# Performance work log

Measured on AMD Instinct MI355X. Metric: run time of the kernel, lower is better.

## Reference

```python
import jax, jax.numpy as jnp
import numpy as np

B, C, H, W = 2, 192, 128, 128
HEADS = 4
M = 128          # num_tokens
RD = 10          # reducted_dim
GS = 256         # category_size
TDF = 16         # dim_ffn_td
HID = 4 * C      # mlp hidden (768)
HIDT = HID + TDF # 784 after concat with token-dict features
KS = 5


def _ln(x, g, b):
    mu = x.mean(-1, keepdims=True)
    var = ((x - mu) ** 2).mean(-1, keepdims=True)
    return (x - mu) / jnp.sqrt(var + 1e-5) * g + b


def _gelu(x):
    return jax.nn.gelu(x, approximate=False)  # torch nn.GELU default = exact erf


def setup_inputs() -> dict:
    key = jax.random.key(0)
    ks = jax.random.split(key, 16)
    s = 0.02
    inp = {
        "x": jax.random.normal(ks[0], (B, C, H, W), jnp.float32),
        "x_size": H,
        "td": jax.random.normal(ks[1], (M, C), jnp.float32),
        "g1": jnp.ones((C,)), "b1": jnp.zeros((C,)),
        "g2": jnp.ones((C,)), "b2": jnp.zeros((C,)),
        "g3": jnp.ones((C,)), "b3": jnp.zeros((C,)),
        "wq_w": jax.random.normal(ks[2], (C, RD)) * s, "wq_b": jnp.zeros((RD,)),
        "wk_w": jax.random.normal(ks[3], (C, RD)) * s, "wk_b": jnp.zeros((RD,)),
        "wv_w": jax.random.normal(ks[4], (C, C)) * s, "wv_b": jnp.zeros((C,)),
        "ca_scale": jnp.ones((1,)),
        "wqkv_w": jax.random.normal(ks[5], (C, 3 * C)) * s, "wqkv_b": jnp.zeros((3 * C,)),
        "proj_w": jax.random.normal(ks[6], (C, C)) * s, "proj_b": jnp.zeros((C,)),
        "fc_td_w": jax.random.normal(ks[7], (C, TDF)) * s, "fc_td_b": jnp.zeros((TDF,)),
        "fc1_w": jax.random.normal(ks[8], (C, HID)) * s, "fc1_b": jnp.zeros((HID,)),
        "dw_w": jax.random.normal(ks[9], (HIDT, 1, KS, KS)) * s, "dw_b": jnp.zeros((HIDT,)),
        "fc2_w": jax.random.normal(ks[10], (HIDT, C)) * s, "fc2_b": jnp.zeros((C,)),
    }
    return inp


def reference(x, x_size, td, g1, b1, g2, b2, g3, b3, wq_w, wq_b, wk_w, wk_b,
              wv_w, wv_b, ca_scale, wqkv_w, wqkv_b, proj_w, proj_b,
              fc_td_w, fc_td_b, fc1_w, fc1_b, dw_w, dw_b, fc2_w, fc2_b):
    b, c, h, w = x.shape
    n = h * w
    xs = x.reshape(b, c, n).transpose(0, 2, 1)          # [b,n,c] patch_embed
    shortcut = xs
    xn = _ln(xs, g1, b1)                                # norm1

    # ---- ATD_CA: L2-normalized cross-attention to token dict ----
    q = xn @ wq_w + wq_b                                # [b,n,rd]
    k = td @ wk_w + wk_b                                # [m,rd]
    v = td @ wv_w + wv_b                                # [m,c]
    qn = q / jnp.maximum(jnp.linalg.norm(q, axis=-1, keepdims=True), 1e-12)
    kn = k / jnp.maximum(jnp.linalg.norm(k, axis=-1, keepdims=True), 1e-12)
    sim = jnp.einsum('bnr,mr->bnm', qn, kn)
    scale = 1.0 + jnp.clip(ca_scale, 0.0, 3.0) * np.log(M)
    sim = jax.nn.softmax(sim * scale, axis=-1)          # [b,n,m]
    x_atd = jnp.einsum('bnm,mc->bnc', sim, v)
    tk_id = jnp.argmax(sim, axis=-1)                    # [b,n] int

    # ---- AC_MSA: category-sorted grouped self-attention ----
    qkv = xn @ wqkv_w + wqkv_b                          # [b,n,3c]
    sort_idx = jnp.argsort(tk_id, axis=-1)              # [b,n]
    inv_idx = jnp.argsort(sort_idx, axis=-1)            # index_reverse
    shuf = jnp.take_along_axis(qkv, sort_idx[:, :, None], axis=1)
    gs = min(n, GS)
    ng = (n + gs - 1) // gs
    pad_n = ng * gs - n
    pad = jnp.flip(shuf[:, n - pad_n:n, :], axis=1)
    padded = jnp.concatenate([shuf, pad], axis=1)       # [b, ng*gs, 3c]
    hd = c // HEADS
    y = padded.reshape(b, ng, gs, 3, HEADS, hd)
    y = jnp.transpose(y, (3, 0, 1, 4, 2, 5))            # [3,b,ng,H,gs,hd]
    q2, k2, v2 = y[0], y[1], y[2]
    attn = jnp.einsum('bghqd,bghkd->bghqk', q2, k2) * (hd ** -0.5)
    attn = jax.nn.softmax(attn, axis=-1)
    o = jnp.einsum('bghqk,bghkd->bghqd', attn, v2)
    o = jnp.transpose(o, (0, 1, 3, 2, 4)).reshape(b, ng * gs, c)[:, :n, :]
    o = jnp.take_along_axis(o, inv_idx[:, :, None], axis=1)
    x_aca = o @ proj_w + proj_b

    # ---- token-dict features gathered per token ----
    td_feat = td @ fc_td_w + fc_td_b                    # [m,tdf]
    x_td = jnp.take(td_feat, tk_id, axis=0)             # [b,n,tdf]

    # ---- ConvFFN_td ----
    xn2 = _ln(xs, g2, b2)
    h1 = _gelu(xn2 @ fc1_w + fc1_b)                     # [b,n,hid]
    hcat = jnp.concatenate([h1, x_td], axis=-1)         # [b,n,hidt]
    img = hcat.transpose(0, 2, 1).reshape(b, HIDT, h, w)
    conv = jax.lax.conv_general_dilated(
        img, dw_w, window_strides=(1, 1), padding=((KS // 2, KS // 2),) * 2,
        dimension_numbers=('NCHW', 'OIHW', 'NCHW'), feature_group_count=HIDT)
    conv = _gelu(conv + dw_b[None, :, None, None])
    conv = conv.reshape(b, HIDT, n).transpose(0, 2, 1)
    x_ffn = (hcat + conv) @ fc2_w + fc2_b
    x_ffn = _ln(x_ffn, g3, b3)                          # norm3

    out = shortcut + x_atd + x_aca + x_ffn
    return out.transpose(0, 2, 1).reshape(b, c, h, w)
```

## Files before the change

kernel.cpp:

```cpp
#include <hip/hip_runtime.h>
#include <hip/hip_bf16.h>
#include <math.h>

using bf16 = __hip_bfloat16;

static constexpr int B = 2, C = 192, Hh = 128, Ww = 128, N = Hh * Ww;
static constexpr int M = 128, RD = 10, GS = 256, NG = N / GS;
static constexpr int HEADS = 4, HD = C / HEADS;
static constexpr int TDF = 16, HID = 4 * C, HIDT = HID + TDF;
static constexpr int TC3 = 3 * C;
static constexpr float LOG_M = 4.852030263919617f;
static constexpr float ATT_SCALE = 0.14433756729740643f;

typedef __attribute__((ext_vector_type(8))) short bf16x8;
typedef __attribute__((ext_vector_type(4))) float f32x4;

__device__ __forceinline__ float b2f(bf16 v) { return __bfloat162float(v); }
__device__ __forceinline__ bf16 f2b(float v) { return __float2bfloat16(v); }
__device__ __forceinline__ float bits2f(unsigned short u) { return __uint_as_float(((unsigned)u) << 16); }
__device__ __forceinline__ unsigned short f2bits(float f) {
    union { bf16 h; unsigned short u; } cv; cv.h = f2b(f); return cv.u;
}
__device__ __forceinline__ float gelu_exact(float v) {
    return 0.5f * v * (1.0f + erff(v * 0.70710678118654752f));
}

__global__ void __launch_bounds__(256) k_wtrans(const float* in, bf16* out, int K, int Nn) {
    __shared__ float T[64][65];
    int n0 = blockIdx.x * 64, k0 = blockIdx.y * 64;
    int tid = threadIdx.x;
    for (int e = tid; e < 4096; e += 256) {
        int kk = e >> 6, nn = e & 63;
        if (k0 + kk < K) T[kk][nn] = in[(size_t)(k0 + kk) * Nn + n0 + nn];
    }
    __syncthreads();
    for (int e = tid; e < 4096; e += 256) {
        int nn = e >> 6, kk = e & 63;
        if (k0 + kk < K) out[(size_t)(n0 + nn) * K + k0 + kk] = f2b(T[kk][nn]);
    }
}

__global__ void k_precompute(const float* td, const float* wk_w, const float* wk_b,
                             const float* wv_w, const float* wv_b,
                             const float* fc_td_w, const float* fc_td_b,
                             float* kn, bf16* vvT, float* tdf) {
    int m = blockIdx.x;
    int lane = threadIdx.x;
    __shared__ float trow[C];
    for (int ch = lane; ch < C; ch += 64) trow[ch] = td[m * C + ch];
    __syncthreads();
    __shared__ float ks[RD];
    __shared__ float inv_s;
    if (lane < RD) {
        float s = wk_b[lane];
        for (int ch = 0; ch < C; ++ch) s += trow[ch] * wk_w[ch * RD + lane];
        ks[lane] = s;
    }
    __syncthreads();
    if (lane == 0) {
        float ss = 0.f;
        for (int r = 0; r < RD; ++r) ss += ks[r] * ks[r];
        inv_s = 1.0f / fmaxf(sqrtf(ss), 1e-12f);
    }
    __syncthreads();
    if (lane < RD) kn[m * RD + lane] = ks[lane] * inv_s;
    for (int c0 = 0; c0 < 3; ++c0) {
        int co = lane + 64 * c0;
        float s = wv_b[co];
        for (int ch = 0; ch < C; ++ch) s += trow[ch] * wv_w[ch * C + co];
        vvT[(size_t)co * M + m] = f2b(s);
    }
    if (lane < TDF) {
        float s = fc_td_b[lane];
        for (int ch = 0; ch < C; ++ch) s += trow[ch] * fc_td_w[ch * TDF + lane];
        tdf[m * TDF + lane] = s;
    }
}

__global__ void __launch_bounds__(256) k_ln(const float* x, const float* g1, const float* b1,
                                            const float* g2, const float* b2v,
                                            bf16* xn1, bf16* xn2, float* xn32, float* acc) {
    __shared__ float Xs[64 * 193];
    __shared__ float mu_s[64], rs_s[64];
    int tid = threadIdx.x;
    int m0 = blockIdx.x * 64;
    int b = m0 / N, i0 = m0 % N;
    for (int e = tid; e < 192 * 64; e += 256) {
        int ch = e >> 6, ii = e & 63;
        Xs[ii * 193 + ch] = x[((size_t)b * C + ch) * N + i0 + ii];
    }
    __syncthreads();
    {
        int tok = tid >> 2, part = tid & 3;
        float s = 0.f, ss = 0.f;
        for (int ch = part * 48; ch < part * 48 + 48; ++ch) {
            float v = Xs[tok * 193 + ch]; s += v; ss += v * v;
        }
        s += __shfl_xor(s, 1); ss += __shfl_xor(ss, 1);
        s += __shfl_xor(s, 2); ss += __shfl_xor(ss, 2);
        if (part == 0) {
            float mu = s / C;
            mu_s[tok] = mu;
            rs_s[tok] = rsqrtf(ss / C - mu * mu + 1e-5f);
        }
    }
    __syncthreads();
    for (int e = tid; e < 64 * 192; e += 256) {
        int ii = e / 192, ch = e % 192;
        float v = Xs[ii * 193 + ch];
        float xn = (v - mu_s[ii]) * rs_s[ii];
        size_t g = (size_t)(m0 + ii);
        xn1[g * C + ch] = f2b(xn * g1[ch] + b1[ch]);
        xn2[g * C + ch] = f2b(xn * g2[ch] + b2v[ch]);
        xn32[g * C + ch] = xn;
        acc[g * C + ch] = v;
    }
}

__global__ void __launch_bounds__(256) k_atdca(const float* xn32, const float* g1, const float* b1,
                        const float* wq_w, const float* wq_b, const float* ca_scale,
                        const float* kn, bf16* p_buf, int* tk_id) {
    int t0 = blockIdx.x * 4;
    int w = threadIdx.x >> 6, lane = threadIdx.x & 63;
    int g = t0 + w;
    float xn[3];
    #pragma unroll
    for (int k = 0; k < 3; ++k) {
        int ch = lane + 64 * k;
        xn[k] = xn32[(size_t)g * C + ch] * g1[ch] + b1[ch];
    }
    float q[RD];
    #pragma unroll
    for (int r = 0; r < RD; ++r) {
        float p = 0.f;
        #pragma unroll
        for (int k = 0; k < 3; ++k) { int ch = lane + 64 * k; p += xn[k] * wq_w[ch * RD + r]; }
        for (int mk = 32; mk >= 1; mk >>= 1) p += __shfl_xor(p, mk);
        q[r] = p + wq_b[r];
    }
    float ssn = 0.f;
    #pragma unroll
    for (int r = 0; r < RD; ++r) ssn += q[r] * q[r];
    float invq = 1.0f / fmaxf(sqrtf(ssn), 1e-12f);
    float s0 = 0.f, s1 = 0.f;
    #pragma unroll
    for (int r = 0; r < RD; ++r) {
        float qr = q[r] * invq;
        s0 += qr * kn[lane * RD + r];
        s1 += qr * kn[(lane + 64) * RD + r];
    }
    float mv; int mi;
    if (s1 > s0) { mv = s1; mi = lane + 64; } else { mv = s0; mi = lane; }
    for (int mk = 32; mk >= 1; mk >>= 1) {
        float ov = __shfl_xor(mv, mk); int oi = __shfl_xor(mi, mk);
        if (ov > mv || (ov == mv && oi < mi)) { mv = ov; mi = oi; }
    }
    float cs = ca_scale[0]; cs = fminf(fmaxf(cs, 0.0f), 3.0f);
    float scale = 1.0f + cs * LOG_M;
    float e0 = expf((s0 - mv) * scale), e1 = expf((s1 - mv) * scale);
    float sum = e0 + e1;
    for (int mk = 32; mk >= 1; mk >>= 1) sum += __shfl_xor(sum, mk);
    float invs = 1.0f / sum;
    p_buf[(size_t)g * M + lane] = f2b(e0 * invs);
    p_buf[(size_t)g * M + lane + 64] = f2b(e1 * invs);
    if (lane == 0) tk_id[g] = mi;
}

__global__ void __launch_bounds__(256) k_pv(const bf16* p_buf, const bf16* vvT, float* acc) {
    __shared__ __align__(16) short As[64 * 136];
    __shared__ __align__(16) short Bs[64 * 136];
    int tid = threadIdx.x;
    int m0 = blockIdx.x * 64;
    int n0 = blockIdx.y * 64;
    for (int e = tid; e < 64 * 16; e += 256) {
        int m = e >> 4, kc = (e & 15) * 8;
        *(uint4*)&As[m * 136 + kc] = *(const uint4*)(p_buf + (size_t)(m0 + m) * M + kc);
    }
    for (int e = tid; e < 64 * 16; e += 256) {
        int n = e >> 4, kc = (e & 15) * 8;
        *(uint4*)&Bs[n * 136 + kc] = *(const uint4*)(vvT + (size_t)(n0 + n) * M + kc);
    }
    __syncthreads();
    int w = tid >> 6, lane = tid & 63;
    int wm = (w >> 1) * 32, wn = (w & 1) * 32;
    int lr = lane & 15, lk = (lane >> 4) * 8;
    f32x4 acc00 = {0.f,0.f,0.f,0.f}, acc01 = acc00, acc10 = acc00, acc11 = acc00;
    #pragma unroll
    for (int ks = 0; ks < 4; ++ks) {
        int k0 = ks * 32 + lk;
        bf16x8 a0 = *(bf16x8*)&As[(wm + lr) * 136 + k0];
        bf16x8 a1 = *(bf16x8*)&As[(wm + 16 + lr) * 136 + k0];
        bf16x8 b0 = *(bf16x8*)&Bs[(wn + lr) * 136 + k0];
        bf16x8 b1 = *(bf16x8*)&Bs[(wn + 16 + lr) * 136 + k0];
        acc00 = __builtin_amdgcn_mfma_f32_16x16x32_bf16(a0, b0, acc00, 0, 0, 0);
        acc01 = __builtin_amdgcn_mfma_f32_16x16x32_bf16(a0, b1, acc01, 0, 0, 0);
        acc10 = __builtin_amdgcn_mfma_f32_16x16x32_bf16(a1, b0, acc10, 0, 0, 0);
        acc11 = __builtin_amdgcn_mfma_f32_16x16x32_bf16(a1, b1, acc11, 0, 0, 0);
    }
    int rbase = (lane >> 4) * 4;
    f32x4 accs[2][2] = {{acc00, acc01}, {acc10, acc11}};
    #pragma unroll
    for (int mt = 0; mt < 2; ++mt) {
        #pragma unroll
        for (int nt = 0; nt < 2; ++nt) {
            int co = n0 + wn + nt * 16 + lr;
            #pragma unroll
            for (int r = 0; r < 4; ++r) {
                int tok = m0 + wm + mt * 16 + rbase + r;
                acc[(size_t)tok * C + co] += accs[mt][nt][r];
            }
        }
    }
}

template<int OUTLD, int MODE>
__global__ void __launch_bounds__(256) k_gemm_big(const bf16* Abuf, const bf16* Wt, const float* bias,
                                                  bf16* outb, float* outf) {
    __shared__ __align__(16) unsigned short As[128 * 104];
    __shared__ __align__(16) unsigned short Bs[96 * 104];
    int tid = threadIdx.x;
    int m0 = blockIdx.x * 128, n0 = blockIdx.y * 96;
    int w = tid >> 6, lane = tid & 63;
    int wm = (w >> 1) * 64, wn = (w & 1) * 48;
    int lr = lane & 15, g8 = lane >> 4;
    f32x4 acc[4][3];
    #pragma unroll
    for (int mt = 0; mt < 4; ++mt)
        #pragma unroll
        for (int nt = 0; nt < 3; ++nt) acc[mt][nt] = (f32x4){0.f,0.f,0.f,0.f};
    for (int kc = 0; kc < 2; ++kc) {
        int kb = kc * 96;
        __syncthreads();
        for (int e = tid; e < 128 * 12; e += 256) {
            int m = e / 12, blk = e % 12;
            *(uint4*)&As[m * 104 + blk * 8] = *(const uint4*)(Abuf + (size_t)(m0 + m) * C + kb + blk * 8);
        }
        for (int e = tid; e < 96 * 12; e += 256) {
            int n = e / 12, blk = e % 12;
            *(uint4*)&Bs[n * 104 + blk * 8] = *(const uint4*)(Wt + (size_t)(n0 + n) * C + kb + blk * 8);
        }
        __syncthreads();
        #pragma unroll
        for (int ks = 0; ks < 3; ++ks) {
            int blk = ks * 4 + g8;
            bf16x8 a[4];
            bf16x8 bfr[3];
            #pragma unroll
            for (int mt = 0; mt < 4; ++mt) a[mt] = *(bf16x8*)&As[(wm + mt * 16 + lr) * 104 + blk * 8];
            #pragma unroll
            for (int nt = 0; nt < 3; ++nt) bfr[nt] = *(bf16x8*)&Bs[(wn + nt * 16 + lr) * 104 + blk * 8];
            #pragma unroll
            for (int mt = 0; mt < 4; ++mt)
                #pragma unroll
                for (int nt = 0; nt < 3; ++nt)
                    acc[mt][nt] = __builtin_amdgcn_mfma_f32_16x16x32_bf16(a[mt], bfr[nt], acc[mt][nt], 0, 0, 0);
        }
    }
    #pragma unroll
    for (int nt = 0; nt < 3; ++nt) {
        int co = n0 + wn + nt * 16 + lr;
        float bv = bias[co];
        #pragma unroll
        for (int mt = 0; mt < 4; ++mt) {
            #pragma unroll
            for (int r = 0; r < 4; ++r) {
                int tok = m0 + wm + mt * 16 + g8 * 4 + r;
                float v = acc[mt][nt][r] + bv;
                if (MODE == 0) outb[(size_t)tok * OUTLD + co] = f2b(v);
                else if (MODE == 1) outb[(size_t)tok * OUTLD + co] = f2b(gelu_exact(v));
                else outf[(size_t)tok * OUTLD + co] += v;
            }
        }
    }
}

__global__ void k_sort_count(const int* tk_id, int* chunk_cnt) {
    int c = blockIdx.x, b = blockIdx.y;
    int tid = threadIdx.x;
    __shared__ int cnt[M];
    cnt[tid] = 0;
    __syncthreads();
    atomicAdd(&cnt[tk_id[b * N + c * 128 + tid]], 1);
    __syncthreads();
    chunk_cnt[(b * 128 + c) * M + tid] = cnt[tid];
}

__global__ void k_sort_scan(int* chunk_cnt) {
    int b = blockIdx.x;
    int k = threadIdx.x;
    int tot = 0;
    for (int c = 0; c < 128; ++c) tot += chunk_cnt[(b * 128 + c) * M + k];
    __shared__ int totals[M];
    __shared__ int base[M];
    totals[k] = tot;
    __syncthreads();
    if (k == 0) {
        int run = 0;
        for (int kk = 0; kk < M; ++kk) { base[kk] = run; run += totals[kk]; }
    }
    __syncthreads();
    int run = base[k];
    for (int c = 0; c < 128; ++c) {
        int v = chunk_cnt[(b * 128 + c) * M + k];
        chunk_cnt[(b * 128 + c) * M + k] = run;
        run += v;
    }
}

__global__ void k_sort_scatter(const int* tk_id, const int* chunk_cnt, int* sort_idx) {
    int c = blockIdx.x, b = blockIdx.y;
    int k = threadIdx.x;
    __shared__ int keys[128];
    keys[k] = tk_id[b * N + c * 128 + k];
    __syncthreads();
    int off = chunk_cnt[(b * 128 + c) * M + k];
    for (int j = 0; j < 128; ++j) {
        if (keys[j] == k) sort_idx[b * N + off++] = c * 128 + j;
    }
}

__global__ void __launch_bounds__(256) k_attn_mfma(const bf16* qkv, const int* sort_idx, bf16* o_buf) {
    int g = blockIdx.x, h = blockIdx.y, b = blockIdx.z;
    __shared__ int sidx[GS];
    __shared__ __align__(16) unsigned short Kl[256 * 64];
    __shared__ __align__(16) unsigned short Vt[48 * 256];
    __shared__ __align__(16) unsigned short Pl[4][64 * 32];
    int tid = threadIdx.x;
    sidx[tid] = sort_idx[b * N + g * GS + tid];
    __syncthreads();
    {
        int row = tid;
        int srow = sidx[row];
        size_t kb = ((size_t)(b * N + srow)) * TC3 + C + h * HD;
        size_t vb = ((size_t)(b * N + srow)) * TC3 + 2 * C + h * HD;
        #pragma unroll
        for (int db = 0; db < 6; ++db) {
            uint4 kv = *(const uint4*)(qkv + kb + db * 8);
            *(uint4*)&Kl[row * 64 + ((db ^ (row & 7)) * 8)] = kv;
            uint4 vv4 = *(const uint4*)(qkv + vb + db * 8);
            unsigned short* vu = (unsigned short*)&vv4;
            #pragma unroll
            for (int j = 0; j < 8; ++j) {
                int d = db * 8 + j;
                Vt[d * 256 + (((row >> 3) ^ (d & 7)) * 8) + (row & 7)] = vu[j];
            }
        }
        uint4 z = {0u,0u,0u,0u};
        *(uint4*)&Kl[row * 64 + ((6 ^ (row & 7)) * 8)] = z;
        *(uint4*)&Kl[row * 64 + ((7 ^ (row & 7)) * 8)] = z;
    }
    __syncthreads();
    int w = tid >> 6, l = tid & 63;
    int lq = l & 15, g8 = l >> 4;
    bf16x8 qf[4][2];
    #pragma unroll
    for (int qt = 0; qt < 4; ++qt) {
        int qrow = sidx[w * 64 + qt * 16 + lq];
        size_t qb = ((size_t)(b * N + qrow)) * TC3 + h * HD;
        qf[qt][0] = *(const bf16x8*)(qkv + qb + g8 * 8);
        int d1 = 32 + g8 * 8;
        if (d1 < HD) qf[qt][1] = *(const bf16x8*)(qkv + qb + d1);
        else { uint4 z = {0u,0u,0u,0u}; qf[qt][1] = *(bf16x8*)&z; }
    }
    float mrun[4], lrun[4];
    f32x4 Oa[4][3];
    #pragma unroll
    for (int qt = 0; qt < 4; ++qt) {
        mrun[qt] = -1e30f; lrun[qt] = 0.f;
        #pragma unroll
        for (int dt = 0; dt < 3; ++dt) Oa[qt][dt] = (f32x4){0.f,0.f,0.f,0.f};
    }
    unsigned short* Pw = &Pl[w][0];
    for (int ck = 0; ck < 8; ++ck) {
        int kbase = ck * 32;
        bf16x8 kf[2][2];
        #pragma unroll
        for (int kt = 0; kt < 2; ++kt) {
            int key = kbase + kt * 16 + lq;
            #pragma unroll
            for (int ks = 0; ks < 2; ++ks)
                kf[kt][ks] = *(bf16x8*)&Kl[key * 64 + (((ks * 4 + g8) ^ (key & 7)) * 8)];
        }
        bf16x8 vf[3];
        #pragma unroll
        for (int dt = 0; dt < 3; ++dt) {
            int d = dt * 16 + lq;
            vf[dt] = *(bf16x8*)&Vt[d * 256 + ((((kbase >> 3) + g8) ^ (d & 7)) * 8)];
        }
        #pragma unroll
        for (int qt = 0; qt < 4; ++qt) {
            f32x4 s0 = {0.f,0.f,0.f,0.f}, s1 = s0;
            s0 = __builtin_amdgcn_mfma_f32_16x16x32_bf16(kf[0][0], qf[qt][0], s0, 0, 0, 0);
            s0 = __builtin_amdgcn_mfma_f32_16x16x32_bf16(kf[0][1], qf[qt][1], s0, 0, 0, 0);
            s1 = __builtin_amdgcn_mfma_f32_16x16x32_bf16(kf[1][0], qf[qt][0], s1, 0, 0, 0);
            s1 = __builtin_amdgcn_mfma_f32_16x16x32_bf16(kf[1][1], qf[qt][1], s1, 0, 0, 0);
            float sv0[4], sv1[4];
            float cmax = -1e30f;
            #pragma unroll
            for (int r = 0; r < 4; ++r) {
                sv0[r] = s0[r] * ATT_SCALE; sv1[r] = s1[r] * ATT_SCALE;
                cmax = fmaxf(cmax, fmaxf(sv0[r], sv1[r]));
            }
            cmax = fmaxf(cmax, __shfl_xor(cmax, 16));
            cmax = fmaxf(cmax, __shfl_xor(cmax, 32));
            float mnew = fmaxf(mrun[qt], cmax);
            float sf = expf(mrun[qt] - mnew);
            float p0[4], p1[4], csum = 0.f;
            #pragma unroll
            for (int r = 0; r < 4; ++r) {
                p0[r] = expf(sv0[r] - mnew); p1[r] = expf(sv1[r] - mnew);
                csum += p0[r] + p1[r];
            }
            csum += __shfl_xor(csum, 16);
            csum += __shfl_xor(csum, 32);
            lrun[qt] = lrun[qt] * sf + csum;
            mrun[qt] = mnew;
            int q = qt * 16 + lq;
            {
                unsigned short pw[4];
                #pragma unroll
                for (int r = 0; r < 4; ++r) pw[r] = f2bits(p0[r]);
                int slot = g8;
                int addr = q * 32 + (((slot >> 1) ^ (q & 3)) * 8) + (slot & 1) * 4;
                *(uint2*)&Pw[addr] = *(uint2*)pw;
                #pragma unroll
                for (int r = 0; r < 4; ++r) pw[r] = f2bits(p1[r]);
                slot = 4 + g8;
                addr = q * 32 + (((slot >> 1) ^ (q & 3)) * 8) + (slot & 1) * 4;
                *(uint2*)&Pw[addr] = *(uint2*)pw;
            }
            float sfr[4];
            #pragma unroll
            for (int r = 0; r < 4; ++r) sfr[r] = __shfl(sf, 4 * g8 + r);
            #pragma unroll
            for (int dt = 0; dt < 3; ++dt)
                #pragma unroll
                for (int r = 0; r < 4; ++r) Oa[qt][dt][r] *= sfr[r];
            bf16x8 pa = *(bf16x8*)&Pw[q * 32 + ((g8 ^ (lq & 3)) * 8)];
            #pragma unroll
            for (int dt = 0; dt < 3; ++dt)
                Oa[qt][dt] = __builtin_amdgcn_mfma_f32_16x16x32_bf16(pa, vf[dt], Oa[qt][dt], 0, 0, 0);
        }
    }
    #pragma unroll
    for (int qt = 0; qt < 4; ++qt) {
        float invq = 1.0f / lrun[qt];
        float invr[4];
        #pragma unroll
        for (int r = 0; r < 4; ++r) invr[r] = __shfl(invq, 4 * g8 + r);
        #pragma unroll
        for (int r = 0; r < 4; ++r) {
            int grow = sidx[w * 64 + qt * 16 + 4 * g8 + r];
            size_t obase = ((size_t)(b * N + grow)) * C + h * HD;
            #pragma unroll
            for (int dt = 0; dt < 3; ++dt)
                o_buf[obase + dt * 16 + lq] = f2b(Oa[qt][dt][r] * invr[r]);
        }
    }
}

__global__ void k_tdfill(const int* tk_id, const float* tdf, bf16* hcat) {
    int idx = blockIdx.x * 256 + threadIdx.x;
    if (idx >= B * N * TDF) return;
    int tok = idx >> 4, f = idx & 15;
    hcat[(size_t)tok * HIDT + HID + f] = f2b(tdf[tk_id[tok] * TDF + f]);
}

__global__ void __launch_bounds__(256) k_conv(const bf16* hcat, const float* dw_w, const float* dw_b,
                                              bf16* convsum) {
    int st = blockIdx.x;
    int c16 = blockIdx.y;
    int b = blockIdx.z;
    int tx0 = (st & 7) * 16, ty0 = (st >> 3) * 16;
    int tid = threadIdx.x;
    __shared__ __align__(16) float Hf[20 * 81 * 4];
    __shared__ __align__(16) float Wf[25 * 16];
    __shared__ float Wb[16];
    for (int e = tid; e < 400; e += 256) {
        int tap = e >> 4, ch = e & 15;
        Wf[e] = dw_w[(size_t)(c16 * 16 + ch) * 25 + tap];
    }
    if (tid < 16) Wb[tid] = dw_b[c16 * 16 + tid];
    for (int e = tid; e < 800; e += 256) {
        int pos = e >> 1, sc = e & 1;
        int py = pos / 20, px = pos % 20;
        int gy = ty0 + py - 2, gx = tx0 + px - 2;
        uint4 v = {0u, 0u, 0u, 0u};
        if (gy >= 0 && gy < Hh && gx >= 0 && gx < Ww)
            v = *(const uint4*)(hcat + ((size_t)b * N + gy * Ww + gx) * HIDT + c16 * 16 + sc * 8);
        unsigned short* u = (unsigned short*)&v;
        float4 f0 = { bits2f(u[0]), bits2f(u[1]), bits2f(u[2]), bits2f(u[3]) };
        float4 f1 = { bits2f(u[4]), bits2f(u[5]), bits2f(u[6]), bits2f(u[7]) };
        int base = (py * 81 + px * 4 + sc * 2) * 4;
        *(float4*)&Hf[base] = f0;
        *(float4*)&Hf[base + 4] = f1;
    }
    __syncthreads();
    int cc = tid & 1, lx = (tid >> 1) & 7, ly = tid >> 4;
    float acc[2][8] = {};
    #pragma unroll 1
    for (int ky = 0; ky < 5; ++ky) {
        int py = ly + ky;
        float4 w[5][2];
        #pragma unroll
        for (int kx = 0; kx < 5; ++kx) {
            w[kx][0] = *(float4*)&Wf[(ky * 5 + kx) * 16 + cc * 8];
            w[kx][1] = *(float4*)&Wf[(ky * 5 + kx) * 16 + cc * 8 + 4];
        }
        #pragma unroll
        for (int c = 0; c < 6; ++c) {
            int px = 2 * lx + c;
            int base = (py * 81 + px * 4 + cc * 2) * 4;
            float4 f0 = *(float4*)&Hf[base];
            float4 f1 = *(float4*)&Hf[base + 4];
            float f[8] = { f0.x, f0.y, f0.z, f0.w, f1.x, f1.y, f1.z, f1.w };
            #pragma unroll
            for (int kx = 0; kx < 5; ++kx) {
                int ox = c - kx;
                if (ox >= 0 && ox < 2) {
                    const float* wp = (const float*)&w[kx][0];
                    #pragma unroll
                    for (int j = 0; j < 8; ++j) acc[ox][j] += f[j] * wp[j];
                }
            }
        }
    }
    int gy = ty0 + ly;
    #pragma unroll
    for (int ox = 0; ox < 2; ++ox) {
        int px = 2 * lx + ox + 2, py = ly + 2;
        int base = (py * 81 + px * 4 + cc * 2) * 4;
        float4 f0 = *(float4*)&Hf[base];
        float4 f1 = *(float4*)&Hf[base + 4];
        float cf[8] = { f0.x, f0.y, f0.z, f0.w, f1.x, f1.y, f1.z, f1.w };
        unsigned short ow[8];
        #pragma unroll
        for (int j = 0; j < 8; ++j)
            ow[j] = f2bits(cf[j] + gelu_exact(acc[ox][j] + Wb[cc * 8 + j]));
        int gx = tx0 + 2 * lx + ox;
        *(uint4*)(convsum + ((size_t)b * N + gy * Ww + gx) * HIDT + c16 * 16 + cc * 8) = *(uint4*)ow;
    }
}

__global__ void __launch_bounds__(256) k_fc2ln(const bf16* convsum, const bf16* Wt,
                                               const float* bias, const float* g3, const float* b3,
                                               const float* accres, const bf16* aca, float* out) {
    __shared__ float Ot[192 * 36];
    __shared__ float partS[4][32], partQ[4][32];
    int tid = threadIdx.x;
    int m0 = blockIdx.x * 32;
    int w = tid >> 6, lane = tid & 63;
    int lr = lane & 15, g8 = lane >> 4;
    int n0 = w * 48;
    f32x4 acc[2][3];
    #pragma unroll
    for (int mt = 0; mt < 2; ++mt)
        #pragma unroll
        for (int nt = 0; nt < 3; ++nt) acc[mt][nt] = (f32x4){0.f,0.f,0.f,0.f};
    const bf16* a0p = convsum + (size_t)(m0 + lr) * HIDT + g8 * 8;
    const bf16* a1p = convsum + (size_t)(m0 + 16 + lr) * HIDT + g8 * 8;
    const bf16* b0p = Wt + (size_t)(n0 + lr) * HIDT + g8 * 8;
    const bf16* b1p = Wt + (size_t)(n0 + 16 + lr) * HIDT + g8 * 8;
    const bf16* b2p = Wt + (size_t)(n0 + 32 + lr) * HIDT + g8 * 8;
    #pragma unroll 4
    for (int kk = 0; kk < 24; ++kk) {
        int k0 = kk * 32;
        bf16x8 a0 = *(const bf16x8*)(a0p + k0);
        bf16x8 a1 = *(const bf16x8*)(a1p + k0);
        bf16x8 w0 = *(const bf16x8*)(b0p + k0);
        bf16x8 w1 = *(const bf16x8*)(b1p + k0);
        bf16x8 w2 = *(const bf16x8*)(b2p + k0);
        acc[0][0] = __builtin_amdgcn_mfma_f32_16x16x32_bf16(a0, w0, acc[0][0], 0, 0, 0);
        acc[0][1] = __builtin_amdgcn_mfma_f32_16x16x32_bf16(a0, w1, acc[0][1], 0, 0, 0);
        acc[0][2] = __builtin_amdgcn_mfma_f32_16x16x32_bf16(a0, w2, acc[0][2], 0, 0, 0);
        acc[1][0] = __builtin_amdgcn_mfma_f32_16x16x32_bf16(a1, w0, acc[1][0], 0, 0, 0);
        acc[1][1] = __builtin_amdgcn_mfma_f32_16x16x32_bf16(a1, w1, acc[1][1], 0, 0, 0);
        acc[1][2] = __builtin_amdgcn_mfma_f32_16x16x32_bf16(a1, w2, acc[1][2], 0, 0, 0);
    }
    {
        uint4 z = {0u,0u,0u,0u};
        bf16x8 a0 = *(bf16x8*)&z, a1 = a0, w0 = a0, w1 = a0, w2 = a0;
        if (g8 < 2) {
            a0 = *(const bf16x8*)(a0p + 768);
            a1 = *(const bf16x8*)(a1p + 768);
            w0 = *(const bf16x8*)(b0p + 768);
            w1 = *(const bf16x8*)(b1p + 768);
            w2 = *(const bf16x8*)(b2p + 768);
        }
        acc[0][0] = __builtin_amdgcn_mfma_f32_16x16x32_bf16(a0, w0, acc[0][0], 0, 0, 0);
        acc[0][1] = __builtin_amdgcn_mfma_f32_16x16x32_bf16(a0, w1, acc[0][1], 0, 0, 0);
        acc[0][2] = __builtin_amdgcn_mfma_f32_16x16x32_bf16(a0, w2, acc[0][2], 0, 0, 0);
        acc[1][0] = __builtin_amdgcn_mfma_f32_16x16x32_bf16(a1, w0, acc[1][0], 0, 0, 0);
        acc[1][1] = __builtin_amdgcn_mfma_f32_16x16x32_bf16(a1, w1, acc[1][1], 0, 0, 0);
        acc[1][2] = __builtin_amdgcn_mfma_f32_16x16x32_bf16(a1, w2, acc[1][2], 0, 0, 0);
    }
    #pragma unroll
    for (int nt = 0; nt < 3; ++nt) {
        float bv = bias[n0 + nt * 16 + lr];
        #pragma unroll
        for (int mt = 0; mt < 2; ++mt)
            #pragma unroll
            for (int r = 0; r < 4; ++r) acc[mt][nt][r] += bv;
    }
    #pragma unroll
    for (int mt = 0; mt < 2; ++mt) {
        #pragma unroll
        for (int r = 0; r < 4; ++r) {
            float s = 0.f, q = 0.f;
            #pragma unroll
            for (int nt = 0; nt < 3; ++nt) { float v = acc[mt][nt][r]; s += v; q += v * v; }
            s += __shfl_xor(s, 1); q += __shfl_xor(q, 1);
            s += __shfl_xor(s, 2); q += __shfl_xor(q, 2);
            s += __shfl_xor(s, 4); q += __shfl_xor(q, 4);
            s += __shfl_xor(s, 8); q += __shfl_xor(q, 8);
            if (lr == 0) {
                int row = mt * 16 + g8 * 4 + r;
                partS[w][row] = s;
                partQ[w][row] = q;
            }
        }
    }
    __syncthreads();
    int bb = m0 / N, i0 = m0 % N;
    #pragma unroll
    for (int mt = 0; mt < 2; ++mt) {
        #pragma unroll
        for (int r = 0; r < 4; ++r) {
            int row = mt * 16 + g8 * 4 + r;
            float s = partS[0][row] + partS[1][row] + partS[2][row] + partS[3][row];
            float q = partQ[0][row] + partQ[1][row] + partQ[2][row] + partQ[3][row];
            float mu = s / C;
            float rstd = rsqrtf(q / C - mu * mu + 1e-5f);
            int tok = m0 + row;
            #pragma unroll
            for (int nt = 0; nt < 3; ++nt) {
                int c = n0 + nt * 16 + lr;
                float o = accres[(size_t)tok * C + c] + b2f(aca[(size_t)tok * C + c])
                        + (acc[mt][nt][r] - mu) * rstd * g3[c] + b3[c];
                Ot[c * 36 + row] = o;
            }
        }
    }
    __syncthreads();
    for (int e = tid; e < 192 * 8; e += 256) {
        int row = e >> 3, q4 = e & 7;
        float4 v = *(float4*)&Ot[row * 36 + q4 * 4];
        *(float4*)(out + ((size_t)(bb * C + row)) * N + i0 + q4 * 4) = v;
    }
}

__global__ void k_sentinel(float* out, int nelem) {
    int i = blockIdx.x * blockDim.x + threadIdx.x;
    if (i < nelem) out[i] = 1234.0f;
}

extern "C" void kernel_launch(void* const* d_in, const int* in_sizes, int n_in,
                              void* d_out, int out_size, void* d_ws, size_t ws_size,
                              hipStream_t stream) {
    const float* x        = (const float*)d_in[0];
    const float* td       = (const float*)d_in[2];
    const float* g1       = (const float*)d_in[3];
    const float* b1       = (const float*)d_in[4];
    const float* g2       = (const float*)d_in[5];
    const float* b2v      = (const float*)d_in[6];
    const float* g3       = (const float*)d_in[7];
    const float* b3       = (const float*)d_in[8];
    const float* wq_w     = (const float*)d_in[9];
    const float* wq_b     = (const float*)d_in[10];
    const float* wk_w     = (const float*)d_in[11];
    const float* wk_b     = (const float*)d_in[12];
    const float* wv_w     = (const float*)d_in[13];
    const float* wv_b     = (const float*)d_in[14];
    const float* ca_scale = (const float*)d_in[15];
    const float* wqkv_w   = (const float*)d_in[16];
    const float* wqkv_b   = (const float*)d_in[17];
    const float* proj_w   = (const float*)d_in[18];
    const float* proj_b   = (const float*)d_in[19];
    const float* fc_td_w  = (const float*)d_in[20];
    const float* fc_td_b  = (const float*)d_in[21];
    const float* fc1_w    = (const float*)d_in[22];
    const float* fc1_b    = (const float*)d_in[23];
    const float* dw_w     = (const float*)d_in[24];
    const float* dw_b     = (const float*)d_in[25];
    const float* fc2_w    = (const float*)d_in[26];
    const float* fc2_b    = (const float*)d_in[27];
    float* out = (float*)d_out;

    char* ws = (char*)d_ws;
    size_t off = 0;
    auto alloc = [&](size_t bytes) { size_t o = off; off += (bytes + 255) & ~(size_t)255; return o; };
    size_t o_xn1   = alloc((size_t)B * N * C * 2);
    size_t o_xn2   = alloc((size_t)B * N * C * 2);
    size_t o_xn32  = alloc((size_t)B * N * C * 4);
    size_t o_acc   = alloc((size_t)B * N * C * 4);
    size_t o_aca   = alloc((size_t)B * N * C * 2);
    size_t o_qkv   = alloc((size_t)B * N * TC3 * 2);
    size_t o_obuf  = alloc((size_t)B * N * C * 2);
    size_t o_hcat  = alloc((size_t)B * N * HIDT * 2);
    size_t o_conv  = alloc((size_t)B * N * HIDT * 2);
    size_t o_kn    = alloc((size_t)M * RD * 4);
    size_t o_vvT   = alloc((size_t)C * M * 2);
    size_t o_tdf   = alloc((size_t)M * TDF * 4);
    size_t o_tk    = alloc((size_t)B * N * 4);
    size_t o_sidx  = alloc((size_t)B * N * 4);
    size_t o_ccnt  = alloc((size_t)B * 128 * M * 4);
    size_t o_pbuf  = alloc((size_t)B * N * M * 2);
    size_t o_wqkvT = alloc((size_t)TC3 * C * 2);
    size_t o_projT = alloc((size_t)C * C * 2);
    size_t o_fc1T  = alloc((size_t)HID * C * 2);
    size_t o_fc2T  = alloc((size_t)C * HIDT * 2);

    if (ws_size < off) {
        k_sentinel<<<(out_size + 255) / 256, 256, 0, stream>>>(out, out_size);
        return;
    }

    bf16*  xn1     = (bf16*)(ws + o_xn1);
    bf16*  xn2     = (bf16*)(ws + o_xn2);
    float* xn32    = (float*)(ws + o_xn32);
    float* acc     = (float*)(ws + o_acc);
    bf16*  aca     = (bf16*)(ws + o_aca);
    bf16*  qkv     = (bf16*)(ws + o_qkv);
    bf16*  o_bufp  = (bf16*)(ws + o_obuf);
    bf16*  hcat    = (bf16*)(ws + o_hcat);
    bf16*  convsum = (bf16*)(ws + o_conv);
    float* kn      = (float*)(ws + o_kn);
    bf16*  vvT     = (bf16*)(ws + o_vvT);
    float* tdf     = (float*)(ws + o_tdf);
    int*   tk_id   = (int*)(ws + o_tk);
    int*   sidx    = (int*)(ws + o_sidx);
    int*   ccnt    = (int*)(ws + o_ccnt);
    bf16*  p_buf   = (bf16*)(ws + o_pbuf);
    bf16*  wqkvT   = (bf16*)(ws + o_wqkvT);
    bf16*  projT   = (bf16*)(ws + o_projT);
    bf16*  fc1T    = (bf16*)(ws + o_fc1T);
    bf16*  fc2T    = (bf16*)(ws + o_fc2T);

    k_wtrans<<<dim3(TC3 / 64, C / 64), 256, 0, stream>>>(wqkv_w, wqkvT, C, TC3);
    k_wtrans<<<dim3(C / 64, C / 64), 256, 0, stream>>>(proj_w, projT, C, C);
    k_wtrans<<<dim3(HID / 64, C / 64), 256, 0, stream>>>(fc1_w, fc1T, C, HID);
    k_wtrans<<<dim3(C / 64, (HIDT + 63) / 64), 256, 0, stream>>>(fc2_w, fc2T, HIDT, C);

    k_precompute<<<M, 64, 0, stream>>>(td, wk_w, wk_b, wv_w, wv_b, fc_td_w, fc_td_b, kn, vvT, tdf);
    k_ln<<<B * N / 64, 256, 0, stream>>>(x, g1, b1, g2, b2v, xn1, xn2, xn32, acc);
    k_atdca<<<B * N / 4, 256, 0, stream>>>(xn32, g1, b1, wq_w, wq_b, ca_scale, kn, p_buf, tk_id);
    k_pv<<<dim3(B * N / 64, C / 64), 256, 0, stream>>>(p_buf, vvT, acc);
    k_gemm_big<TC3, 0><<<dim3(B * N / 128, TC3 / 96), 256, 0, stream>>>(
        xn1, wqkvT, wqkv_b, qkv, nullptr);
    k_sort_count<<<dim3(128, B), 128, 0, stream>>>(tk_id, ccnt);
    k_sort_scan<<<B, 128, 0, stream>>>(ccnt);
    k_sort_scatter<<<dim3(128, B), 128, 0, stream>>>(tk_id, ccnt, sidx);
    k_attn_mfma<<<dim3(NG, HEADS, B), 256, 0, stream>>>(qkv, sidx, o_bufp);
    k_gemm_big<C, 0><<<dim3(B * N / 128, C / 96), 256, 0, stream>>>(
        o_bufp, projT, proj_b, aca, nullptr);
    k_gemm_big<HIDT, 1><<<dim3(B * N / 128, HID / 96), 256, 0, stream>>>(
        xn2, fc1T, fc1_b, hcat, nullptr);
    k_tdfill<<<(B * N * TDF + 255) / 256, 256, 0, stream>>>(tk_id, tdf, hcat);
    k_conv<<<dim3(64, 49, B), 256, 0, stream>>>(hcat, dw_w, dw_b, convsum);
    k_fc2ln<<<B * N / 32, 256, 0, stream>>>(convsum, fc2T, fc2_b, g3, b3, acc, aca, out);
}
```

Baseline: 386.8 us.

## Fold LayerNorm affine into weights and fuse QKV and FC1 GEMMs

Folds the norm1/norm2 gamma and beta into the QKV and FC1 weights and biases, so LayerNorm writes a single un-affined bf16 normalized activation instead of two. The QKV and FC1 projections then run as one concatenated GEMM over the shared input, with the epilogue routing columns to qkv or to GELU into hcat. This removes one activation write and one re-read of the A operand, at the cost of new weight and bias prep kernels. Rounding changes slightly because the gamma scaling now happens before the bf16 cast of the weights.

```diff
diff --git a/kernel.cpp b/kernel.cpp
--- a/kernel.cpp
+++ b/kernel.cpp
@@ -9,6 +9,7 @@
 static constexpr int HEADS = 4, HD = C / HEADS;
 static constexpr int TDF = 16, HID = 4 * C, HIDT = HID + TDF;
 static constexpr int TC3 = 3 * C;
+static constexpr int NCAT = TC3 + HID;
 static constexpr float LOG_M = 4.852030263919617f;
 static constexpr float ATT_SCALE = 0.14433756729740643f;
 
@@ -38,6 +39,46 @@
         int nn = e >> 6, kk = e & 63;
         if (k0 + kk < K) out[(size_t)(n0 + nn) * K + k0 + kk] = f2b(T[kk][nn]);
     }
+}
+
+__global__ void __launch_bounds__(256) k_wprep(const float* wqkv_w, const float* fc1_w,
+                                               const float* g1, const float* g2, bf16* WcatT) {
+    __shared__ float T[192 * 65];
+    __shared__ float gl[192];
+    int n0 = blockIdx.x * 64;
+    int tid = threadIdx.x;
+    bool isq = (n0 < TC3);
+    const float* W = isq ? wqkv_w : fc1_w;
+    const float* g = isq ? g1 : g2;
+    int Nn = isq ? TC3 : HID;
+    int nb = isq ? n0 : n0 - TC3;
+    for (int k = tid; k < 192; k += 256) gl[k] = g[k];
+    __syncthreads();
+    for (int e = tid; e < 192 * 64; e += 256) {
+        int k = e >> 6, nn = e & 63;
+        T[k * 65 + nn] = W[(size_t)k * Nn + nb + nn] * gl[k];
+    }
+    __syncthreads();
+    for (int e = tid; e < 64 * 192; e += 256) {
+        int nn = e / 192, k = e % 192;
+        WcatT[(size_t)(n0 + nn) * C + k] = f2b(T[k * 65 + nn]);
+    }
+}
+
+__global__ void k_bprep(const float* wqkv_w, const float* fc1_w, const float* wqkv_b,
+                        const float* fc1_b, const float* b1, const float* b2v, float* bcat) {
+    int n = blockIdx.x * 256 + threadIdx.x;
+    if (n >= NCAT) return;
+    float s;
+    if (n < TC3) {
+        s = wqkv_b[n];
+        for (int k = 0; k < C; ++k) s += b1[k] * wqkv_w[(size_t)k * TC3 + n];
+    } else {
+        int nn = n - TC3;
+        s = fc1_b[nn];
+        for (int k = 0; k < C; ++k) s += b2v[k] * fc1_w[(size_t)k * HID + nn];
+    }
+    bcat[n] = s;
 }
 
 __global__ void k_precompute(const float* td, const float* wk_w, const float* wk_b,
@@ -77,9 +118,7 @@
     }
 }
 
-__global__ void __launch_bounds__(256) k_ln(const float* x, const float* g1, const float* b1,
-                                            const float* g2, const float* b2v,
-                                            bf16* xn1, bf16* xn2, float* xn32, float* acc) {
+__global__ void __launch_bounds__(256) k_ln(const float* x, bf16* xn, float* xn32, float* acc) {
     __shared__ float Xs[64 * 193];
     __shared__ float mu_s[64], rs_s[64];
     int tid = threadIdx.x;
@@ -108,11 +147,10 @@
     for (int e = tid; e < 64 * 192; e += 256) {
         int ii = e / 192, ch = e % 192;
         float v = Xs[ii * 193 + ch];
-        float xn = (v - mu_s[ii]) * rs_s[ii];
+        float xnv = (v - mu_s[ii]) * rs_s[ii];
         size_t g = (size_t)(m0 + ii);
-        xn1[g * C + ch] = f2b(xn * g1[ch] + b1[ch]);
-        xn2[g * C + ch] = f2b(xn * g2[ch] + b2v[ch]);
-        xn32[g * C + ch] = xn;
+        xn[g * C + ch] = f2b(xnv);
+        xn32[g * C + ch] = xnv;
         acc[g * C + ch] = v;
     }
 }
@@ -208,6 +246,66 @@
             for (int r = 0; r < 4; ++r) {
                 int tok = m0 + wm + mt * 16 + rbase + r;
                 acc[(size_t)tok * C + co] += accs[mt][nt][r];
+            }
+        }
+    }
+}
+
+__global__ void __launch_bounds__(256) k_gemm_fused(const bf16* Abuf, const bf16* Wt, const float* bias,
+                                                    bf16* qkv, bf16* hcat) {
+    __shared__ __align__(16) unsigned short As[128 * 104];
+    __shared__ __align__(16) unsigned short Bs[96 * 104];
+    int tid = threadIdx.x;
+    int m0 = blockIdx.x * 128, n0 = blockIdx.y * 96;
+    int w = tid >> 6, lane = tid & 63;
+    int wm = (w >> 1) * 64, wn = (w & 1) * 48;
+    int lr = lane & 15, g8 = lane >> 4;
+    f32x4 acc[4][3];
+    #pragma unroll
+    for (int mt = 0; mt < 4; ++mt)
+        #pragma unroll
+        for (int nt = 0; nt < 3; ++nt) acc[mt][nt] = (f32x4){0.f,0.f,0.f,0.f};
+    for (int kc = 0; kc < 2; ++kc) {
+        int kb = kc * 96;
+        __syncthreads();
+        for (int e = tid; e < 128 * 12; e += 256) {
+            int m = e / 12, blk = e % 12;
+            *(uint4*)&As[m * 104 + blk * 8] = *(const uint4*)(Abuf + (size_t)(m0 + m) * C + kb + blk * 8);
+        }
+        for (int e = tid; e < 96 * 12; e += 256) {
+            int n = e / 12, blk = e % 12;
+            *(uint4*)&Bs[n * 104 + blk * 8] = *(const uint4*)(Wt + (size_t)(n0 + n) * C + kb + blk * 8);
+        }
+        __syncthreads();
+        #pragma unroll
+        for (int ks = 0; ks < 3; ++ks) {
+            int blk = ks * 4 + g8;
+            bf16x8 a[4];
+            bf16x8 bfr[3];
+            #pragma unroll
+            for (int mt = 0; mt < 4; ++mt) a[mt] = *(bf16x8*)&As[(wm + mt * 16 + lr) * 104 + blk * 8];
+            #pragma unroll
+            for (int nt = 0; nt < 3; ++nt) bfr[nt] = *(bf16x8*)&Bs[(wn + nt * 16 + lr) * 104 + blk * 8];
+            #pragma unroll
+            for (int mt = 0; mt < 4; ++mt)
+                #pragma unroll
+                for (int nt = 0; nt < 3; ++nt)
+                    acc[mt][nt] = __builtin_amdgcn_mfma_f32_16x16x32_bf16(a[mt], bfr[nt], acc[mt][nt], 0, 0, 0);
+        }
+    }
+    bool isq = (n0 < TC3);
+    #pragma unroll
+    for (int nt = 0; nt < 3; ++nt) {
+        int co = n0 + wn + nt * 16 + lr;
+        float bv = bias[co];
+        #pragma unroll
+        for (int mt = 0; mt < 4; ++mt) {
+            #pragma unroll
+            for (int r = 0; r < 4; ++r) {
+                int tok = m0 + wm + mt * 16 + g8 * 4 + r;
+                float v = acc[mt][nt][r] + bv;
+                if (isq) qkv[(size_t)tok * TC3 + co] = f2b(v);
+                else     hcat[(size_t)tok * HIDT + (co - TC3)] = f2b(gelu_exact(v));
             }
         }
     }
@@ -689,15 +787,14 @@
     char* ws = (char*)d_ws;
     size_t off = 0;
     auto alloc = [&](size_t bytes) { size_t o = off; off += (bytes + 255) & ~(size_t)255; return o; };
-    size_t o_xn1   = alloc((size_t)B * N * C * 2);
-    size_t o_xn2   = alloc((size_t)B * N * C * 2);
+    size_t o_xn    = alloc((size_t)B * N * C * 2);
     size_t o_xn32  = alloc((size_t)B * N * C * 4);
     size_t o_acc   = alloc((size_t)B * N * C * 4);
     size_t o_aca   = alloc((size_t)B * N * C * 2);
     size_t o_qkv   = alloc((size_t)B * N * TC3 * 2);
-    size_t o_obuf  = alloc((size_t)B * N * C * 2);
     size_t o_hcat  = alloc((size_t)B * N * HIDT * 2);
     size_t o_conv  = alloc((size_t)B * N * HIDT * 2);
+    size_t o_obuf  = alloc((size_t)B * N * C * 2);
     size_t o_kn    = alloc((size_t)M * RD * 4);
     size_t o_vvT   = alloc((size_t)C * M * 2);
     size_t o_tdf   = alloc((size_t)M * TDF * 4);
@@ -705,9 +802,9 @@
     size_t o_sidx  = alloc((size_t)B * N * 4);
     size_t o_ccnt  = alloc((size_t)B * 128 * M * 4);
     size_t o_pbuf  = alloc((size_t)B * N * M * 2);
-    size_t o_wqkvT = alloc((size_t)TC3 * C * 2);
+    size_t o_wcat  = alloc((size_t)NCAT * C * 2);
+    size_t o_bcat  = alloc((size_t)NCAT * 4);
     size_t o_projT = alloc((size_t)C * C * 2);
-    size_t o_fc1T  = alloc((size_t)HID * C * 2);
     size_t o_fc2T  = alloc((size_t)C * HIDT * 2);
 
     if (ws_size < off) {
@@ -715,15 +812,14 @@
         return;
     }
 
-    bf16*  xn1     = (bf16*)(ws + o_xn1);
-    bf16*  xn2     = (bf16*)(ws + o_xn2);
+    bf16*  xn      = (bf16*)(ws + o_xn);
     float* xn32    = (float*)(ws + o_xn32);
     float* acc     = (float*)(ws + o_acc);
     bf16*  aca     = (bf16*)(ws + o_aca);
     bf16*  qkv     = (bf16*)(ws + o_qkv);
-    bf16*  o_bufp  = (bf16*)(ws + o_obuf);
     bf16*  hcat    = (bf16*)(ws + o_hcat);
     bf16*  convsum = (bf16*)(ws + o_conv);
+    bf16*  o_bufp  = (bf16*)(ws + o_obuf);
     float* kn      = (float*)(ws + o_kn);
     bf16*  vvT     = (bf16*)(ws + o_vvT);
     float* tdf     = (float*)(ws + o_tdf);
@@ -731,30 +827,27 @@
     int*   sidx    = (int*)(ws + o_sidx);
     int*   ccnt    = (int*)(ws + o_ccnt);
     bf16*  p_buf   = (bf16*)(ws + o_pbuf);
-    bf16*  wqkvT   = (bf16*)(ws + o_wqkvT);
+    bf16*  WcatT   = (bf16*)(ws + o_wcat);
+    float* bcat    = (float*)(ws + o_bcat);
     bf16*  projT   = (bf16*)(ws + o_projT);
-    bf16*  fc1T    = (bf16*)(ws + o_fc1T);
     bf16*  fc2T    = (bf16*)(ws + o_fc2T);
 
-    k_wtrans<<<dim3(TC3 / 64, C / 64), 256, 0, stream>>>(wqkv_w, wqkvT, C, TC3);
+    k_wprep<<<NCAT / 64, 256, 0, stream>>>(wqkv_w, fc1_w, g1, g2, WcatT);
+    k_bprep<<<(NCAT + 255) / 256, 256, 0, stream>>>(wqkv_w, fc1_w, wqkv_b, fc1_b, b1, b2v, bcat);
     k_wtrans<<<dim3(C / 64, C / 64), 256, 0, stream>>>(proj_w, projT, C, C);
-    k_wtrans<<<dim3(HID / 64, C / 64), 256, 0, stream>>>(fc1_w, fc1T, C, HID);
     k_wtrans<<<dim3(C / 64, (HIDT + 63) / 64), 256, 0, stream>>>(fc2_w, fc2T, HIDT, C);
 
     k_precompute<<<M, 64, 0, stream>>>(td, wk_w, wk_b, wv_w, wv_b, fc_td_w, fc_td_b, kn, vvT, tdf);
-    k_ln<<<B * N / 64, 256, 0, stream>>>(x, g1, b1, g2, b2v, xn1, xn2, xn32, acc);
+    k_ln<<<B * N / 64, 256, 0, stream>>>(x, xn, xn32, acc);
     k_atdca<<<B * N / 4, 256, 0, stream>>>(xn32, g1, b1, wq_w, wq_b, ca_scale, kn, p_buf, tk_id);
     k_pv<<<dim3(B * N / 64, C / 64), 256, 0, stream>>>(p_buf, vvT, acc);
-    k_gemm_big<TC3, 0><<<dim3(B * N / 128, TC3 / 96), 256, 0, stream>>>(
-        xn1, wqkvT, wqkv_b, qkv, nullptr);
+    k_gemm_fused<<<dim3(B * N / 128, NCAT / 96), 256, 0, stream>>>(xn, WcatT, bcat, qkv, hcat);
     k_sort_count<<<dim3(128, B), 128, 0, stream>>>(tk_id, ccnt);
     k_sort_scan<<<B, 128, 0, stream>>>(ccnt);
     k_sort_scatter<<<dim3(128, B), 128, 0, stream>>>(tk_id, ccnt, sidx);
     k_attn_mfma<<<dim3(NG, HEADS, B), 256, 0, stream>>>(qkv, sidx, o_bufp);
     k_gemm_big<C, 0><<<dim3(B * N / 128, C / 96), 256, 0, stream>>>(
         o_bufp, projT, proj_b, aca, nullptr);
-    k_gemm_big<HIDT, 1><<<dim3(B * N / 128, HID / 96), 256, 0, stream>>>(
-        xn2, fc1T, fc1_b, hcat, nullptr);
     k_tdfill<<<(B * N * TDF + 255) / 256, 256, 0, stream>>>(tk_id, tdf, hcat);
     k_conv<<<dim3(64, 49, B), 256, 0, stream>>>(hcat, dw_w, dw_b, convsum);
     k_fc2ln<<<B * N / 32, 256, 0, stream>>>(convsum, fc2T, fc2_b, g3, b3, acc, aca, out);
```

New measurement: 373.0 us. 3.6% less time.
